# Optimization experiments

Hardware: AMD Instinct MI355X
Metric: run time of the kernel (lower is better)

## Reference

```python
import jax, jax.numpy as jnp
import numpy as np

E, M, IN, OUT = 8, 8192, 2048, 8192


def setup_inputs() -> dict:
    key = jax.random.key(0)
    k1, k2, k3 = jax.random.split(key, 3)
    inputs = jax.random.normal(k1, (M, IN), dtype=jnp.float32)
    # truncated_normal(-3,3) scaled by init_scale/sqrt(In), matching MoELinear.init
    weight = jax.random.truncated_normal(k2, -3.0, 3.0, (E, IN, OUT), dtype=jnp.float32) * (1.0 / np.sqrt(IN))
    bias = jax.random.normal(k3, (OUT,), dtype=jnp.float32) * 0.02
    # tokens are pre-sorted by expert; balanced routing: M/E tokens per expert
    group_sizes = jnp.full((E,), M // E, dtype=jnp.int32)
    return {"inputs": inputs, "weight": weight, "group_sizes": group_sizes, "bias": bias}


def _ragged_matmul(inputs, weight, group_sizes):
    """Grouped GEMM: out[m] = inputs[m] @ weight[expert_of(m)].

    Tokens are contiguous per expert; group_sizes[e] gives the count for
    expert e. Same math as jax.lax.ragged_dot / megablox gmm.
    """
    n_experts = weight.shape[0]
    m = inputs.shape[0]
    # static-length repeat -> per-token expert id, jit-safe
    expert_ids = jnp.repeat(jnp.arange(n_experts, dtype=group_sizes.dtype),
                            group_sizes, total_repeat_length=m)  # [M]

    def body(acc, ew):
        e, w = ew  # w: [In, Out]
        mask = (expert_ids == e).astype(inputs.dtype)  # [M]
        return acc + (inputs * mask[:, None]) @ w, None

    acc0 = jnp.zeros((m, weight.shape[2]), dtype=inputs.dtype)
    out, _ = jax.lax.scan(body, acc0, (jnp.arange(n_experts, dtype=group_sizes.dtype), weight))
    return out


def reference(inputs, weight, group_sizes, bias):
    # MoELinear.__call__ (ragged_dot path): grouped matmul + bias
    return _ragged_matmul(inputs, weight, group_sizes) + bias
```

## Files before the change

kernel.cpp:

```cpp
#include <hip/hip_runtime.h>
#include <stdint.h>

#define E_ 8
#define M_ 8192
#define K_ 2048
#define N_ 8192

#define BM 256
#define BN 256
#define BK 64
#define NT (K_ / BK)
#define LDS_BYTES 131072

typedef __attribute__((ext_vector_type(8))) short bf16x8;
typedef __attribute__((ext_vector_type(4))) float f32x4;
typedef __attribute__((ext_vector_type(8))) unsigned short us8;

__device__ __forceinline__ unsigned short f2bf(float f) {
  union { float f; uint32_t u; } v; v.f = f;
  uint32_t u = v.u;
  uint32_t r = (u + 0x7FFFu + ((u >> 16) & 1u)) >> 16;
  return (unsigned short)r;
}

__device__ __forceinline__ void gload_lds16(const void* g, void* l) {
  __builtin_amdgcn_global_load_lds(
      (const __attribute__((address_space(1))) unsigned int*)g,
      (__attribute__((address_space(3))) unsigned int*)l,
      16, 0, 0);
}

__global__ __launch_bounds__(256) void conv_a(const float* __restrict__ A,
                                              unsigned short* __restrict__ Ab,
                                              int n8) {
  int stride = gridDim.x * blockDim.x;
  for (int idx = blockIdx.x * blockDim.x + threadIdx.x; idx < n8; idx += stride) {
    const float4* p = reinterpret_cast<const float4*>(A) + (size_t)idx * 2;
    float4 x0 = p[0], x1 = p[1];
    us8 o;
    o[0] = f2bf(x0.x); o[1] = f2bf(x0.y); o[2] = f2bf(x0.z); o[3] = f2bf(x0.w);
    o[4] = f2bf(x1.x); o[5] = f2bf(x1.y); o[6] = f2bf(x1.z); o[7] = f2bf(x1.w);
    *reinterpret_cast<us8*>(Ab + (size_t)idx * 8) = o;
  }
}

__global__ __launch_bounds__(256) void conv_wT(const float* __restrict__ W,
                                               unsigned short* __restrict__ Wt,
                                               int e_fixed) {
  __shared__ float t[64][65];
  int tid = threadIdx.x;
  int tx = tid & 63, ty = tid >> 6;
  int n0 = blockIdx.x * 64, k0 = blockIdx.y * 64;
  int e = (gridDim.z > 1) ? blockIdx.z : e_fixed;
  size_t win = (size_t)e * K_ * N_;
  size_t wout = (gridDim.z > 1) ? win : 0;

  #pragma unroll
  for (int r = 0; r < 16; ++r) {
    int kl = r * 4 + ty;
    t[kl][tx] = W[win + (size_t)(k0 + kl) * N_ + n0 + tx];
  }
  __syncthreads();
  int px = tid & 31, py = tid >> 5;
  #pragma unroll
  for (int r = 0; r < 8; ++r) {
    int nl = r * 8 + py;
    unsigned int pack = (unsigned int)f2bf(t[2 * px][nl]) |
                        ((unsigned int)f2bf(t[2 * px + 1][nl]) << 16);
    *reinterpret_cast<unsigned int*>(Wt + wout + (size_t)(n0 + nl) * K_ + k0 + 2 * px) = pack;
  }
}

__global__ __launch_bounds__(512, 2) void moe_gemm_bf16(
    const unsigned short* __restrict__ Ab,
    const unsigned short* __restrict__ Wt,
    const int* __restrict__ gs,
    const float* __restrict__ bias,
    float* __restrict__ C,
    int only_expert, size_t wt_stride) {
  extern __shared__ char smem[];

  int tile_n = blockIdx.x;
  int tile_m = blockIdx.y;

  int expert = -1, row_start = 0, rows = 0;
  if (only_expert >= 0) {
    int off = 0;
    for (int e = 0; e < only_expert; ++e) off += gs[e];
    int g = gs[only_expert];
    int t0 = tile_m * BM;
    if (t0 >= g) return;
    expert = only_expert;
    row_start = off + t0;
    rows = min(BM, g - t0);
  } else {
    int acc = 0, off = 0;
    for (int e = 0; e < E_; ++e) {
      int g = gs[e];
      int t = (g + BM - 1) / BM;
      if (expert < 0 && tile_m < acc + t) {
        int lt = tile_m - acc;
        expert = e;
        row_start = off + lt * BM;
        rows = min(BM, g - lt * BM);
      }
      acc += t;
      off += g;
    }
    if (expert < 0) return;
  }

  const unsigned short* WtE = Wt + (size_t)expert * wt_stride;

  int tid = threadIdx.x;
  int lane = tid & 63;
  int wave = tid >> 6;
  int wr = wave >> 2;
  int wc = wave & 3;
  int bh = wc >> 1;
  int ln15 = lane & 15;
  int n0 = tile_n * BN;

  int sl16 = (((lane >> 4) ^ ((ln15 & 3) ^ ((ln15 >> 2) & 3))) << 4);
  int aRB = wr * 16384 + ln15 * 64 + sl16;
  int bRB = 32768 + bh * 16384 + ((wc & 1) * 64 + ln15) * 64 + sl16;

  int soff = tid * 16;
  int srow = soff >> 6;
  int sslot = (soff >> 4) & 3;
  int skc = sslot ^ ((srow & 3) ^ ((srow >> 2) & 3));
  int scol0 = skc * 8;

  const unsigned short* aS[2][2];
  const unsigned short* bS[2][2];
  #pragma unroll
  for (int h = 0; h < 2; ++h) {
    int r = h * 128 + srow;
    int gr = r < rows ? r : 0;
    #pragma unroll
    for (int ks = 0; ks < 2; ++ks) {
      aS[h][ks] = Ab + (size_t)(row_start + gr) * K_ + ks * 32 + scol0;
      bS[h][ks] = WtE + (size_t)(n0 + h * 128 + srow) * K_ + ks * 32 + scol0;
    }
  }

#define STG_A(DB, h, ks, kt) \
  gload_lds16(aS[h][ks] + (kt) * 64, smem + (DB) + (h) * 16384 + (ks) * 8192 + soff)
#define STG_B(DB, h, ks, kt) \
  gload_lds16(bS[h][ks] + (kt) * 64, smem + (DB) + 32768 + (h) * 16384 + (ks) * 8192 + soff)

  f32x4 acc4[8][4];
  #pragma unroll
  for (int i = 0; i < 8; ++i)
    #pragma unroll
    for (int j = 0; j < 4; ++j)
      acc4[i][j] = f32x4{0.f, 0.f, 0.f, 0.f};

#define DS_A(frag, DB, KS, MIBASE)                                            \
  _Pragma("unroll") for (int mi = 0; mi < 4; ++mi)                            \
    frag[mi] = *(const bf16x8*)(smem + (DB) + aRB + (KS) * 8192 +             \
                                ((MIBASE) + mi) * 1024);
#define DS_B(frag, DB, KS)                                                    \
  _Pragma("unroll") for (int nj = 0; nj < 4; ++nj)                            \
    frag[nj] = *(const bf16x8*)(smem + (DB) + bRB + (KS) * 8192 + nj * 1024);
#define MFMA16(MB, af, bf)                                                    \
  __builtin_amdgcn_s_setprio(1);                                              \
  _Pragma("unroll") for (int mi = 0; mi < 4; ++mi)                            \
    _Pragma("unroll") for (int nj = 0; nj < 4; ++nj)                          \
      acc4[(MB) + mi][nj] = __builtin_amdgcn_mfma_f32_16x16x32_bf16(          \
          af[mi], bf[nj], acc4[(MB) + mi][nj], 0, 0, 0);                      \
  __builtin_amdgcn_s_setprio(0);

#define TILE4(DB, DBN, KTN)                                                   \
  do {                                                                        \
    bf16x8 af[4], bf[4];                                                      \
                                              \
    DS_A(af, DB, 0, 0); DS_B(bf, DB, 0);                                      \
    STG_A(DBN, 0, 0, KTN); STG_B(DBN, 0, 0, KTN);                             \
    __builtin_amdgcn_s_barrier();                                             \
    asm volatile("s_waitcnt lgkmcnt(0)" ::: "memory");                        \
    __builtin_amdgcn_sched_barrier(0);                                        \
    MFMA16(0, af, bf);                                                        \
    __builtin_amdgcn_s_barrier();                                             \
                                    \
    DS_A(af, DB, 0, 4);                                                       \
    STG_A(DBN, 1, 0, KTN); STG_B(DBN, 1, 0, KTN);                             \
    __builtin_amdgcn_s_barrier();                                             \
    asm volatile("s_waitcnt lgkmcnt(0)" ::: "memory");                        \
    __builtin_amdgcn_sched_barrier(0);                                        \
    MFMA16(4, af, bf);                                                        \
    asm volatile("s_waitcnt vmcnt(4)" ::: "memory");                          \
    __builtin_amdgcn_s_barrier();                                             \
                                              \
    DS_A(af, DB, 1, 0); DS_B(bf, DB, 1);                                      \
    STG_A(DBN, 0, 1, KTN); STG_B(DBN, 0, 1, KTN);                             \
    __builtin_amdgcn_s_barrier();                                             \
    asm volatile("s_waitcnt lgkmcnt(0)" ::: "memory");                        \
    __builtin_amdgcn_sched_barrier(0);                                        \
    MFMA16(0, af, bf);                                                        \
    __builtin_amdgcn_s_barrier();                                             \
                                                       \
    DS_A(af, DB, 1, 4);                                                       \
    STG_A(DBN, 1, 1, KTN); STG_B(DBN, 1, 1, KTN);                             \
    __builtin_amdgcn_s_barrier();                                             \
    asm volatile("s_waitcnt lgkmcnt(0)" ::: "memory");                        \
    __builtin_amdgcn_sched_barrier(0);                                        \
    MFMA16(4, af, bf);                                                        \
    asm volatile("s_waitcnt vmcnt(4)" ::: "memory");                          \
    __builtin_amdgcn_s_barrier();                                             \
  } while (0)

  STG_A(0, 0, 0, 0); STG_B(0, 0, 0, 0);
  STG_A(0, 1, 0, 0); STG_B(0, 1, 0, 0);
  STG_A(0, 0, 1, 0); STG_B(0, 0, 1, 0);
  STG_A(0, 1, 1, 0); STG_B(0, 1, 1, 0);
  asm volatile("s_waitcnt vmcnt(4)" ::: "memory");
  __builtin_amdgcn_s_barrier();

  for (int t2 = 0; t2 < NT; t2 += 2) {
    int ktn2 = (t2 + 2 >= NT) ? 0 : t2 + 2;
    TILE4(0, 65536, t2 + 1);
    TILE4(65536, 0, ktn2);
  }
#undef TILE4
#undef DS_A
#undef DS_B
#undef MFMA16
#undef STG_A
#undef STG_B

  asm volatile("s_waitcnt vmcnt(0)" ::: "memory");

  float bv[4];
  #pragma unroll
  for (int nj = 0; nj < 4; ++nj) bv[nj] = bias[n0 + wc * 64 + nj * 16 + ln15];
  #pragma unroll
  for (int mi = 0; mi < 8; ++mi) {
    int r0 = wr * 128 + mi * 16 + (lane >> 4) * 4;
    #pragma unroll
    for (int r = 0; r < 4; ++r) {
      int lr = r0 + r;
      if (lr < rows) {
        float* Cp = C + (size_t)(row_start + lr) * N_ + n0 + wc * 64 + ln15;
        #pragma unroll
        for (int nj = 0; nj < 4; ++nj) Cp[nj * 16] = acc4[mi][nj][r] + bv[nj];
      }
    }
  }
}

__global__ __launch_bounds__(256) void moe_naive(const float* __restrict__ A,
                                                 const float* __restrict__ W,
                                                 const int* __restrict__ gs,
                                                 const float* __restrict__ bias,
                                                 float* __restrict__ C) {
  int col = blockIdx.x * 16 + (threadIdx.x & 15);
  int row = blockIdx.y * 16 + (threadIdx.x >> 4);
  int acc = 0, e = E_ - 1;
  for (int i = 0; i < E_; ++i) {
    int g = gs[i];
    if (row >= acc && row < acc + g) { e = i; break; }
    acc += g;
  }
  const float* a = A + (size_t)row * K_;
  const float* w = W + (size_t)e * K_ * N_ + col;
  float s = 0.f;
  for (int k = 0; k < K_; ++k) s += a[k] * w[(size_t)k * N_];
  C[(size_t)row * N_ + col] = s + bias[col];
}

extern "C" void kernel_launch(void* const* d_in, const int* in_sizes, int n_in,
                              void* d_out, int out_size, void* d_ws, size_t ws_size,
                              hipStream_t stream) {
  const float* A = (const float*)d_in[0];
  const float* W = (const float*)d_in[1];
  const int* gs = (const int*)d_in[2];
  const float* bias = (const float*)d_in[3];
  float* C = (float*)d_out;

  const size_t needA = (size_t)M_ * K_ * 2;
  const size_t needWall = (size_t)E_ * K_ * N_ * 2;
  const size_t needW1 = (size_t)K_ * N_ * 2;

  (void)hipFuncSetAttribute((const void*)moe_gemm_bf16,
                            hipFuncAttributeMaxDynamicSharedMemorySize, LDS_BYTES);

  if (ws_size >= needA + needWall) {
    unsigned short* Abf = (unsigned short*)d_ws;
    unsigned short* Wtb = (unsigned short*)((char*)d_ws + needA);
    conv_a<<<2048, 256, 0, stream>>>(A, Abf, (M_ * K_) / 8);
    dim3 gw(N_ / 64, K_ / 64, E_);
    conv_wT<<<gw, 256, 0, stream>>>(W, Wtb, 0);
    dim3 gg(N_ / BN, M_ / BM + E_);
    moe_gemm_bf16<<<gg, 512, LDS_BYTES, stream>>>(Abf, Wtb, gs, bias, C, -1, (size_t)N_ * K_);
  } else if (ws_size >= needA + needW1) {
    unsigned short* Abf = (unsigned short*)d_ws;
    unsigned short* Wtb = (unsigned short*)((char*)d_ws + needA);
    conv_a<<<2048, 256, 0, stream>>>(A, Abf, (M_ * K_) / 8);
    for (int e = 0; e < E_; ++e) {
      dim3 gw(N_ / 64, K_ / 64, 1);
      conv_wT<<<gw, 256, 0, stream>>>(W, Wtb, e);
      dim3 gg(N_ / BN, M_ / BM);
      moe_gemm_bf16<<<gg, 512, LDS_BYTES, stream>>>(Abf, Wtb, gs, bias, C, e, 0);
    }
  } else {
    dim3 gn(N_ / 16, M_ / 16);
    moe_naive<<<gn, 256, 0, stream>>>(A, W, gs, bias, C);
  }
}
```

Measured before the change: 460.0 us.

## Change LDS tile layout to full-row 128-byte rows with XOR-8 swizzle

```diff
diff --git a/kernel.cpp b/kernel.cpp
--- a/kernel.cpp
+++ b/kernel.cpp
@@ -121,33 +121,29 @@
   int ln15 = lane & 15;
   int n0 = tile_n * BN;
 
-  int sl16 = (((lane >> 4) ^ ((ln15 & 3) ^ ((ln15 >> 2) & 3))) << 4);
-  int aRB = wr * 16384 + ln15 * 64 + sl16;
-  int bRB = 32768 + bh * 16384 + ((wc & 1) * 64 + ln15) * 64 + sl16;
+  int slot0 = (((lane >> 4) ^ (ln15 & 7)) << 4);
+  int aBase = wr * 16384 + ln15 * 128;
+  int bBase = 32768 + bh * 16384 + (wc & 1) * 8192 + ln15 * 128;
 
   int soff = tid * 16;
-  int srow = soff >> 6;
-  int sslot = (soff >> 4) & 3;
-  int skc = sslot ^ ((srow & 3) ^ ((srow >> 2) & 3));
-  int scol0 = skc * 8;
-
-  const unsigned short* aS[2][2];
-  const unsigned short* bS[2][2];
-  #pragma unroll
-  for (int h = 0; h < 2; ++h) {
-    int r = h * 128 + srow;
+  int crow = tid >> 3;
+  int lslot = (tid & 7) ^ (crow & 7);
+  int scol = lslot * 8;
+
+  const unsigned short* aS[4];
+  const unsigned short* bS[4];
+  #pragma unroll
+  for (int c = 0; c < 4; ++c) {
+    int r = c * 64 + crow;
     int gr = r < rows ? r : 0;
-    #pragma unroll
-    for (int ks = 0; ks < 2; ++ks) {
-      aS[h][ks] = Ab + (size_t)(row_start + gr) * K_ + ks * 32 + scol0;
-      bS[h][ks] = WtE + (size_t)(n0 + h * 128 + srow) * K_ + ks * 32 + scol0;
-    }
-  }
-
-#define STG_A(DB, h, ks, kt) \
-  gload_lds16(aS[h][ks] + (kt) * 64, smem + (DB) + (h) * 16384 + (ks) * 8192 + soff)
-#define STG_B(DB, h, ks, kt) \
-  gload_lds16(bS[h][ks] + (kt) * 64, smem + (DB) + 32768 + (h) * 16384 + (ks) * 8192 + soff)
+    aS[c] = Ab + (size_t)(row_start + gr) * K_ + scol;
+    bS[c] = WtE + (size_t)(n0 + r) * K_ + scol;
+  }
+
+#define STG_A(DB, c, kt) \
+  gload_lds16(aS[c] + (kt) * 64, smem + (DB) + (c) * 8192 + soff)
+#define STG_B(DB, c, kt) \
+  gload_lds16(bS[c] + (kt) * 64, smem + (DB) + 32768 + (c) * 8192 + soff)
 
   f32x4 acc4[8][4];
   #pragma unroll
@@ -156,13 +152,14 @@
     for (int j = 0; j < 4; ++j)
       acc4[i][j] = f32x4{0.f, 0.f, 0.f, 0.f};
 
-#define DS_A(frag, DB, KS, MIBASE)                                            \
+#define DS_A(frag, DB, MH, KS)                                                \
   _Pragma("unroll") for (int mi = 0; mi < 4; ++mi)                            \
-    frag[mi] = *(const bf16x8*)(smem + (DB) + aRB + (KS) * 8192 +             \
-                                ((MIBASE) + mi) * 1024);
+    frag[mi] = *(const bf16x8*)(smem + (DB) + aBase + (MH) * 8192 +           \
+                                mi * 2048 + (slot0 ^ ((KS) << 6)));
 #define DS_B(frag, DB, KS)                                                    \
   _Pragma("unroll") for (int nj = 0; nj < 4; ++nj)                            \
-    frag[nj] = *(const bf16x8*)(smem + (DB) + bRB + (KS) * 8192 + nj * 1024);
+    frag[nj] = *(const bf16x8*)(smem + (DB) + bBase + nj * 2048 +             \
+                                (slot0 ^ ((KS) << 6)));
 #define MFMA16(MB, af, bf)                                                    \
   __builtin_amdgcn_s_setprio(1);                                              \
   _Pragma("unroll") for (int mi = 0; mi < 4; ++mi)                            \
@@ -174,53 +171,52 @@
 #define TILE4(DB, DBN, KTN)                                                   \
   do {                                                                        \
     bf16x8 af[4], bf[4];                                                      \
-                                              \
+                                                                      \
     DS_A(af, DB, 0, 0); DS_B(bf, DB, 0);                                      \
-    STG_A(DBN, 0, 0, KTN); STG_B(DBN, 0, 0, KTN);                             \
+    STG_B(DBN, 0, KTN); STG_B(DBN, 1, KTN);                                   \
     __builtin_amdgcn_s_barrier();                                             \
     asm volatile("s_waitcnt lgkmcnt(0)" ::: "memory");                        \
     __builtin_amdgcn_sched_barrier(0);                                        \
     MFMA16(0, af, bf);                                                        \
-    __builtin_amdgcn_s_barrier();                                             \
-                                    \
-    DS_A(af, DB, 0, 4);                                                       \
-    STG_A(DBN, 1, 0, KTN); STG_B(DBN, 1, 0, KTN);                             \
+    asm volatile("s_waitcnt vmcnt(2)" ::: "memory");                          \
+    __builtin_amdgcn_s_barrier();                                             \
+                                                   \
+    DS_A(af, DB, 1, 0);                                                       \
+    STG_B(DBN, 2, KTN); STG_B(DBN, 3, KTN);                                   \
     __builtin_amdgcn_s_barrier();                                             \
     asm volatile("s_waitcnt lgkmcnt(0)" ::: "memory");                        \
     __builtin_amdgcn_sched_barrier(0);                                        \
     MFMA16(4, af, bf);                                                        \
-    asm volatile("s_waitcnt vmcnt(4)" ::: "memory");                          \
-    __builtin_amdgcn_s_barrier();                                             \
-                                              \
-    DS_A(af, DB, 1, 0); DS_B(bf, DB, 1);                                      \
-    STG_A(DBN, 0, 1, KTN); STG_B(DBN, 0, 1, KTN);                             \
+    __builtin_amdgcn_s_barrier();                                             \
+                                                                      \
+    DS_A(af, DB, 0, 1); DS_B(bf, DB, 1);                                      \
+    STG_A(DBN, 0, KTN); STG_A(DBN, 2, KTN);                                   \
     __builtin_amdgcn_s_barrier();                                             \
     asm volatile("s_waitcnt lgkmcnt(0)" ::: "memory");                        \
     __builtin_amdgcn_sched_barrier(0);                                        \
     MFMA16(0, af, bf);                                                        \
     __builtin_amdgcn_s_barrier();                                             \
-                                                       \
-    DS_A(af, DB, 1, 4);                                                       \
-    STG_A(DBN, 1, 1, KTN); STG_B(DBN, 1, 1, KTN);                             \
+                                                                      \
+    DS_A(af, DB, 1, 1);                                                       \
+    STG_A(DBN, 1, KTN); STG_A(DBN, 3, KTN);                                   \
     __builtin_amdgcn_s_barrier();                                             \
     asm volatile("s_waitcnt lgkmcnt(0)" ::: "memory");                        \
     __builtin_amdgcn_sched_barrier(0);                                        \
     MFMA16(4, af, bf);                                                        \
-    asm volatile("s_waitcnt vmcnt(4)" ::: "memory");                          \
+    asm volatile("s_waitcnt vmcnt(2)" ::: "memory");                          \
     __builtin_amdgcn_s_barrier();                                             \
   } while (0)
 
-  STG_A(0, 0, 0, 0); STG_B(0, 0, 0, 0);
-  STG_A(0, 1, 0, 0); STG_B(0, 1, 0, 0);
-  STG_A(0, 0, 1, 0); STG_B(0, 0, 1, 0);
-  STG_A(0, 1, 1, 0); STG_B(0, 1, 1, 0);
-  asm volatile("s_waitcnt vmcnt(4)" ::: "memory");
+  STG_B(0, 0, 0); STG_B(0, 1, 0); STG_B(0, 2, 0); STG_B(0, 3, 0);
+  STG_A(0, 0, 0); STG_A(0, 2, 0);
+  STG_A(0, 1, 0); STG_A(0, 3, 0);
+  asm volatile("s_waitcnt vmcnt(2)" ::: "memory");
   __builtin_amdgcn_s_barrier();
 
   for (int t2 = 0; t2 < NT; t2 += 2) {
-    int ktn2 = (t2 + 2 >= NT) ? 0 : t2 + 2;
+    int k2 = (t2 + 2 >= NT) ? 0 : t2 + 2;
     TILE4(0, 65536, t2 + 1);
-    TILE4(65536, 0, ktn2);
+    TILE4(65536, 0, k2);
   }
 #undef TILE4
 #undef DS_A
```

New measurement: 428.3 us. 1.07x faster.
